# Kernel tuning notes

Measured on AMD Instinct MI355X. Metric: run time of the kernel, lower is better.

The kernel has to match this reference:

```python
import jax, jax.numpy as jnp
import numpy as np

NATTRS, NOBJS = 250, 400
N = NATTRS + NOBJS           # 650 graph nodes
E = 100000                   # edges
D_IN, D_HID, D_NODE = 512, 4096, 512
FEAT, EMB, B = 2048, 800, 256
LN_EPS = 1e-5


def setup_inputs() -> dict:
    key = jax.random.key(0)
    ks = jax.random.split(key, 32)
    w = lambda k, shape: (jax.random.normal(k, shape, jnp.float32) / np.sqrt(shape[-1])).astype(jnp.float32)
    return {
        'img': jax.random.normal(ks[0], (B, FEAT), jnp.float32),
        'nodes': jax.random.normal(ks[1], (N, D_IN), jnp.float32),
        'edge_src': jax.random.randint(ks[2], (E,), 0, N),
        'edge_dst': jax.random.randint(ks[3], (E,), 0, N),
        'W1l': w(ks[4], (D_HID, D_IN)), 'b1': jnp.zeros((D_HID,), jnp.float32), 'W1r': w(ks[5], (D_HID, D_IN)),
        'W2l': w(ks[6], (D_NODE, D_HID)), 'b2': jnp.zeros((D_NODE,), jnp.float32), 'W2r': w(ks[7], (D_NODE, D_HID)),
        'Wp1': w(ks[8], (1200, 2 * D_NODE)), 'bp1': jnp.zeros((1200,), jnp.float32),
        'Wp2': w(ks[9], (EMB, 1200)), 'bp2': jnp.zeros((EMB,), jnp.float32),
        'gp': jnp.ones((EMB,), jnp.float32), 'bpn': jnp.zeros((EMB,), jnp.float32),
        'Wi1': w(ks[10], (768, FEAT)), 'bi1': jnp.zeros((768,), jnp.float32),
        'Wi2': w(ks[11], (1000, 768)), 'bi2': jnp.zeros((1000,), jnp.float32),
        'Wi3': w(ks[12], (EMB, 1000)), 'bi3': jnp.zeros((EMB,), jnp.float32),
        'gi': jnp.ones((EMB,), jnp.float32), 'bin_': jnp.zeros((EMB,), jnp.float32),
    }


def _segment_mean(x, src, dst, n):
    # gather source features, mean-aggregate at destinations (PyG SAGEConv 'mean')
    agg = jax.ops.segment_sum(x[src], dst, num_segments=n)
    deg = jax.ops.segment_sum(jnp.ones_like(dst, dtype=x.dtype), dst, num_segments=n)
    return agg / jnp.clip(deg, 1.0)[:, None]


def _sage(x, src, dst, Wl, bl, Wr):
    # out_i = lin_l(mean_{j in N(i)} x_j) + lin_r(x_i); lin_r has no bias in PyG
    return _segment_mean(x, src, dst, x.shape[0]) @ Wl.T + bl + x @ Wr.T


def _ln(x, g, b):
    m = x.mean(-1, keepdims=True)
    v = ((x - m) ** 2).mean(-1, keepdims=True)
    return (x - m) / jnp.sqrt(v + LN_EPS) * g + b


def reference(img, nodes, edge_src, edge_dst, W1l, b1, W1r, W2l, b2, W2r,
              Wp1, bp1, Wp2, bp2, gp, bpn, Wi1, bi1, Wi2, bi2, Wi3, bi3, gi, bin_):
    # GCN backbone (dropout is identity in eval)
    h = jax.nn.relu(_sage(nodes, edge_src, edge_dst, W1l, b1, W1r))
    out_nodes = _sage(h, edge_src, edge_dst, W2l, b2, W2r)          # [N, 512]
    # all attr-obj pairs: attr repeated per obj, objs tiled per attr
    attr = out_nodes[:NATTRS]
    obj = out_nodes[NATTRS:]
    pa = jnp.repeat(attr, NOBJS, axis=0)                            # [P, 512]
    po = jnp.tile(obj, (NATTRS, 1))                                 # [P, 512]
    pairs = jnp.concatenate([pa, po], axis=1)                       # [P, 1024]
    # pair_fc: Linear-ReLU -> Linear -> LayerNorm
    p = jax.nn.relu(pairs @ Wp1.T + bp1)
    p = _ln(p @ Wp2.T + bp2, gp, bpn)                               # [P, 800]
    # img_fc: two hidden Linear-ReLU -> Linear -> LayerNorm
    i = jax.nn.relu(img @ Wi1.T + bi1)
    i = jax.nn.relu(i @ Wi2.T + bi2)
    i = _ln(i @ Wi3.T + bi3, gi, bin_)                              # [B, 800]
    return i @ p.T                                                  # [B, P]
```

## Files before the change

### kernel.cpp

```cpp
#include <hip/hip_runtime.h>

#define NN 650
#define NE 100000

typedef short bf16x8_t __attribute__((ext_vector_type(8)));
typedef short s16x4_t __attribute__((ext_vector_type(4)));
typedef float f32x4_t __attribute__((ext_vector_type(4)));

__device__ __forceinline__ unsigned short f2bf(float f) {
  union { float f; unsigned u; } x; x.f = f;
  unsigned r = x.u + 0x7fffu + ((x.u >> 16) & 1u);
  return (unsigned short)(r >> 16);
}
__device__ __forceinline__ float bf2f(unsigned short u) {
  union { unsigned u; float f; } x; x.u = ((unsigned)u) << 16; return x.f;
}

typedef const __attribute__((address_space(1))) unsigned int* gptr_t;
typedef __attribute__((address_space(3))) unsigned int* lptr_t;
__device__ __forceinline__ void gl_lds16(const unsigned short* g, unsigned short* l) {
  __builtin_amdgcn_global_load_lds((gptr_t)g, (lptr_t)l, 16, 0, 0);
}

__global__ void k_scatter(const int* __restrict__ src, const int* __restrict__ dst,
                          float* __restrict__ C, float* __restrict__ deg) {
  int e = blockIdx.x * 256 + threadIdx.x;
  if (e < NE) {
    int s = src[e], d = dst[e];
    atomicAdd(&C[d * NN + s], 1.0f);
    atomicAdd(&deg[d], 1.0f);
  }
}

__global__ void k_adj_norm(const float* __restrict__ C, const float* __restrict__ deg,
                           unsigned short* __restrict__ Cn) {
  int idx = blockIdx.x * 256 + threadIdx.x;
  if (idx >= 768 * 672) return;
  int i = idx / 672, j = idx - i * 672;
  float v = (i < NN && j < NN) ? C[i * NN + j] / fmaxf(deg[i], 1.0f) : 0.0f;
  Cn[idx] = f2bf(v);
}

#define MAXJ 12
struct CvtDesc { const float* src; unsigned short* dst; int Mvalid, Kin, ldi, off, ldo, nElem, nblk; };
struct CvtPack { CvtDesc d[MAXJ]; };
__global__ void k_cvt_all(CvtPack P) {
  int b = blockIdx.x;
  int j = 0;
  while (b >= P.d[j].nblk) { b -= P.d[j].nblk; ++j; }
  const CvtDesc D = P.d[j];
  int idx = b * 256 + threadIdx.x;
  if (idx >= D.nElem) return;
  int r = idx / D.ldo, c = idx - r * D.ldo;
  D.dst[idx] = (r < D.Mvalid && c < D.Kin) ? f2bf(D.src[(size_t)r * D.ldi + D.off + c]) : (unsigned short)0;
}

__global__ void k_ttr(const unsigned short* __restrict__ in, unsigned short* __restrict__ out,
                      int ldi, int ldo) {
  __shared__ unsigned short tile[64][65];
  const int c0 = blockIdx.x * 64, r0 = blockIdx.y * 64;
  const int t = threadIdx.x;
  const int rl = t >> 4, cl = (t & 15) * 4;
#pragma unroll
  for (int rr = 0; rr < 4; ++rr) {
    s16x4_t v = *(const s16x4_t*)(in + (size_t)(r0 + rl + rr * 16) * ldi + c0 + cl);
#pragma unroll
    for (int j = 0; j < 4; ++j) tile[rl + rr * 16][cl + j] = (unsigned short)v[j];
  }
  __syncthreads();
  if (r0 + cl < ldo) {
#pragma unroll
    for (int cc = 0; cc < 4; ++cc) {
      int crow = rl + cc * 16;
      unsigned short o[4] = { tile[cl + 0][crow], tile[cl + 1][crow],
                              tile[cl + 2][crow], tile[cl + 3][crow] };
      *(s16x4_t*)(out + (size_t)(c0 + crow) * ldo + r0 + cl) = *(s16x4_t*)o;
    }
  }
}

__global__ void k_pgen(const float* __restrict__ Pa, const float* __restrict__ Po,
                       unsigned short* __restrict__ P, int r0, int rows) {
  int g = blockIdx.x * 256 + threadIdx.x;
  if (g >= rows * 152) return;
  int lp = g / 152, k = (g - lp * 152) * 8;
  int p = r0 + lp;
  unsigned short t8[8];
  if (p < 100000) {
    int a = p / 400, o = p - a * 400;
    const float* pa = Pa + (size_t)a * 1216 + k;
    const float* po = Po + (size_t)o * 1216 + k;
    float4 x1 = *(const float4*)(pa);
    float4 x2 = *(const float4*)(pa + 4);
    float4 y1 = *(const float4*)(po);
    float4 y2 = *(const float4*)(po + 4);
    t8[0] = f2bf(fmaxf(x1.x + y1.x, 0.f)); t8[1] = f2bf(fmaxf(x1.y + y1.y, 0.f));
    t8[2] = f2bf(fmaxf(x1.z + y1.z, 0.f)); t8[3] = f2bf(fmaxf(x1.w + y1.w, 0.f));
    t8[4] = f2bf(fmaxf(x2.x + y2.x, 0.f)); t8[5] = f2bf(fmaxf(x2.y + y2.y, 0.f));
    t8[6] = f2bf(fmaxf(x2.z + y2.z, 0.f)); t8[7] = f2bf(fmaxf(x2.w + y2.w, 0.f));
  } else {
#pragma unroll
    for (int j = 0; j < 8; ++j) t8[j] = 0;
  }
  *(bf16x8_t*)(P + (size_t)lp * 1216 + k) = *(bf16x8_t*)t8;
}

__global__ void k_stats_fin(float* __restrict__ S, float* __restrict__ SS) {
  int i = blockIdx.x * 256 + threadIdx.x;
  if (i >= 100096) return;
  float s = S[i], ss = SS[i];
  float m = s * (1.0f / 800.0f);
  float var = ss * (1.0f / 800.0f) - m * m;
  S[i] = m;
  SS[i] = rsqrtf(fmaxf(var, 0.f) + 1e-5f);
}

__global__ void k_prep_i(const unsigned short* __restrict__ iB,
                         const float* __restrict__ gp, const float* __restrict__ bpn,
                         unsigned short* __restrict__ iG,
                         float* __restrict__ c1, float* __restrict__ c2) {
  const int row = blockIdx.x, t = threadIdx.x;
  float s1 = 0.f, s2 = 0.f;
  if (t < 100) {
    bf16x8_t v = *(const bf16x8_t*)(iB + (size_t)row * 800 + t * 8);
    unsigned short o[8];
#pragma unroll
    for (int j = 0; j < 8; ++j) {
      float f = bf2f((unsigned short)v[j]);
      float g = gp[t * 8 + j];
      s1 += f * g; s2 += f * bpn[t * 8 + j];
      o[j] = f2bf(f * g);
    }
    *(bf16x8_t*)(iG + (size_t)row * 800 + t * 8) = *(bf16x8_t*)o;
  }
#pragma unroll
  for (int off = 32; off > 0; off >>= 1) { s1 += __shfl_down(s1, off); s2 += __shfl_down(s2, off); }
  __shared__ float sh[4];
  int w = t >> 6, lane = t & 63;
  if (lane == 0) { sh[w] = s1; sh[2 + w] = s2; }
  __syncthreads();
  if (t == 0) { c1[row] = sh[0] + sh[1]; c2[row] = sh[2] + sh[3]; }
}

#define BK 32
template<int OUT_BF, int RELU, int LNF, int QST>
__launch_bounds__(256)
__global__ void k_gemm128(const unsigned short* __restrict__ A,
                          const unsigned short* __restrict__ B,
                          const float* __restrict__ bias,
                          const float* __restrict__ addb,
                          void* __restrict__ Cout,
                          int K, int ldc,
                          int Mvalid, int Nvalid, int Nstore, int swap, int swz,
                          const float* __restrict__ lnm, const float* __restrict__ lninv,
                          const float* __restrict__ lnc1, const float* __restrict__ lnc2,
                          float* __restrict__ sumP, float* __restrict__ ssP) {
  __shared__ unsigned short As[2][128 * BK];
  __shared__ unsigned short Bs[2][128 * BK];
  const int tid = threadIdx.x;
  const int w = tid >> 6, lane = tid & 63;
  int bx = blockIdx.x, by = blockIdx.y;
  if (swz) {
    int T = gridDim.x * gridDim.y;
    int flat = blockIdx.x + gridDim.x * blockIdx.y;
    int xcd = flat & 7, s = flat >> 3;
    int qq = T >> 3, rr = T & 7;
    int slot = (xcd < rr ? xcd * (qq + 1) : rr * (qq + 1) + (xcd - rr) * qq) + s;
    bx = slot % gridDim.x; by = slot / gridDim.x;
  }
  const int bm = swap ? by : bx;
  const int bn = swap ? bx : by;
  const int m0 = bm * 128, n0 = bn * 128;
  const int wm = w & 1, wn = w >> 1;
  const int lr = lane & 15, q = lane >> 4;

  const int srow = w * 32 + (lane >> 2);
  const int scol = (lane & 3) * 8;
  const unsigned short* Ag = A + (size_t)(m0 + srow) * K + scol;
  const unsigned short* Bg = B + (size_t)(n0 + srow) * K + scol;
  const int so0 = (w * 32) * BK;
  const int so1 = (w * 32 + 16) * BK;

  f32x4_t acc[4][4];
#pragma unroll
  for (int r = 0; r < 4; ++r)
#pragma unroll
    for (int t = 0; t < 4; ++t) { f32x4_t z = {0.f, 0.f, 0.f, 0.f}; acc[r][t] = z; }

  const int nt = K / BK;
  gl_lds16(Ag, &As[0][so0]); gl_lds16(Ag + 16 * (size_t)K, &As[0][so1]);
  gl_lds16(Bg, &Bs[0][so0]); gl_lds16(Bg + 16 * (size_t)K, &Bs[0][so1]);
  Ag += BK; Bg += BK;

  for (int t = 0; t < nt; ++t) {
    const int cur = t & 1;
    __syncthreads();
    if (t + 1 < nt) {
      const int nxt = cur ^ 1;
      gl_lds16(Ag, &As[nxt][so0]); gl_lds16(Ag + 16 * (size_t)K, &As[nxt][so1]);
      gl_lds16(Bg, &Bs[nxt][so0]); gl_lds16(Bg + 16 * (size_t)K, &Bs[nxt][so1]);
      Ag += BK; Bg += BK;
    }
    bf16x8_t af[4], bfv[4];
#pragma unroll
    for (int r = 0; r < 4; ++r)
      af[r] = *(const bf16x8_t*)(&As[cur][(wm * 64 + r * 16 + lr) * BK + q * 8]);
#pragma unroll
    for (int tt = 0; tt < 4; ++tt)
      bfv[tt] = *(const bf16x8_t*)(&Bs[cur][(wn * 64 + tt * 16 + lr) * BK + q * 8]);
#pragma unroll
    for (int r = 0; r < 4; ++r)
#pragma unroll
      for (int tt = 0; tt < 4; ++tt)
        acc[r][tt] = __builtin_amdgcn_mfma_f32_16x16x32_bf16(af[r], bfv[tt], acc[r][tt], 0, 0, 0);
  }

  if (QST) {
#pragma unroll
    for (int r = 0; r < 4; ++r) {
#pragma unroll
      for (int e = 0; e < 4; ++e) {
        const int gm = m0 + wm * 64 + r * 16 + q * 4 + e;
        float s = 0.f, ss = 0.f;
#pragma unroll
        for (int t = 0; t < 4; ++t) {
          const int gn = n0 + wn * 64 + t * 16 + lr;
          float v = 0.f;
          if (gm < Mvalid && gn < Nvalid) v = acc[r][t][e] + bias[gn];
          if (gn < Nstore)
            ((unsigned short*)Cout)[(size_t)gm * ldc + gn] = f2bf(v);
          s += v; ss += v * v;
        }
#pragma unroll
        for (int m = 1; m < 16; m <<= 1) {
          s += __shfl_xor(s, m);
          ss += __shfl_xor(ss, m);
        }
        if (lr == 0 && gm < Mvalid) {
          atomicAdd(&sumP[gm], s);
          atomicAdd(&ssP[gm], ss);
        }
      }
    }
  } else {
#pragma unroll
    for (int r = 0; r < 4; ++r) {
#pragma unroll
      for (int t = 0; t < 4; ++t) {
#pragma unroll
        for (int e = 0; e < 4; ++e) {
          int gm = m0 + wm * 64 + r * 16 + q * 4 + e;
          int gn = n0 + wn * 64 + t * 16 + lr;
          if (gn < Nstore) {
            float v = 0.f;
            if (gm < Mvalid && gn < Nvalid) {
              v = acc[r][t][e];
              if (LNF) {
                v = lninv[gn] * (v - lnm[gn] * lnc1[gm]) + lnc2[gm];
              } else {
                if (bias) v += bias[gn];
                if (addb) v += addb[(size_t)gm * ldc + gn];
                if (RELU) v = fmaxf(v, 0.f);
              }
            }
            if (OUT_BF) ((unsigned short*)Cout)[(size_t)gm * ldc + gn] = f2bf(v);
            else        ((float*)Cout)[(size_t)gm * ldc + gn] = v;
          }
        }
      }
    }
  }
}

__global__ void k_ln_img(const float* __restrict__ in, unsigned short* __restrict__ out,
                         const float* __restrict__ g, const float* __restrict__ b) {
  const int row = blockIdx.x, t = threadIdx.x;
  float v[4]; float s = 0.f, ss = 0.f; int j = 0;
  for (int idx = t; idx < 800; idx += 256, ++j) {
    float x = in[(size_t)row * 800 + idx];
    v[j] = x; s += x; ss += x * x;
  }
#pragma unroll
  for (int off = 32; off > 0; off >>= 1) {
    s += __shfl_down(s, off);
    ss += __shfl_down(ss, off);
  }
  __shared__ float sh[8];
  int wave = t >> 6, lane = t & 63;
  if (lane == 0) { sh[wave] = s; sh[4 + wave] = ss; }
  __syncthreads();
  if (t == 0) {
    float S = sh[0] + sh[1] + sh[2] + sh[3];
    float SS = sh[4] + sh[5] + sh[6] + sh[7];
    float m = S * (1.0f / 800.0f);
    float var = SS * (1.0f / 800.0f) - m * m;
    sh[0] = m; sh[1] = rsqrtf(fmaxf(var, 0.f) + 1e-5f);
  }
  __syncthreads();
  float m = sh[0], inv = sh[1];
  j = 0;
  for (int idx = t; idx < 800; idx += 256, ++j) {
    float y = (v[j] - m) * inv * g[idx] + b[idx];
    out[(size_t)row * 800 + idx] = f2bf(y);
  }
}

extern "C" void kernel_launch(void* const* d_in, const int* in_sizes, int n_in,
                              void* d_out, int out_size, void* d_ws, size_t ws_size,
                              hipStream_t stream) {
  (void)in_sizes; (void)n_in; (void)out_size; (void)ws_size;
  const float* img  = (const float*)d_in[0];
  const float* nodes= (const float*)d_in[1];
  const int* esrc   = (const int*)d_in[2];
  const int* edst   = (const int*)d_in[3];
  const float* W1l  = (const float*)d_in[4];
  const float* b1   = (const float*)d_in[5];
  const float* W1r  = (const float*)d_in[6];
  const float* W2l  = (const float*)d_in[7];
  const float* b2   = (const float*)d_in[8];
  const float* W2r  = (const float*)d_in[9];
  const float* Wp1  = (const float*)d_in[10];
  const float* bp1  = (const float*)d_in[11];
  const float* Wp2  = (const float*)d_in[12];
  const float* bp2  = (const float*)d_in[13];
  const float* gp   = (const float*)d_in[14];
  const float* bpn  = (const float*)d_in[15];
  const float* Wi1  = (const float*)d_in[16];
  const float* bi1  = (const float*)d_in[17];
  const float* Wi2  = (const float*)d_in[18];
  const float* bi2  = (const float*)d_in[19];
  const float* Wi3  = (const float*)d_in[20];
  const float* bi3  = (const float*)d_in[21];
  const float* gi   = (const float*)d_in[22];
  const float* binp = (const float*)d_in[23];

  char* wsp = (char*)d_ws;
  auto alloc = [&](size_t bytes) -> void* {
    void* p = (void*)wsp; wsp += (bytes + 255) & ~(size_t)255; return p;
  };
  unsigned short* onB    = (unsigned short*)alloc((size_t)768 * 512 * 2);
  unsigned short* Wp1LB  = (unsigned short*)alloc((size_t)1280 * 512 * 2);
  unsigned short* Wp1RB  = (unsigned short*)alloc((size_t)1280 * 512 * 2);
  unsigned short* Wp2B   = (unsigned short*)alloc((size_t)896 * 1216 * 2);
  float* PaB             = (float*)alloc((size_t)256 * 1216 * 4);
  float* PoB             = (float*)alloc((size_t)512 * 1216 * 4);
  unsigned short* imgB   = (unsigned short*)alloc((size_t)256 * 2048 * 2);
  unsigned short* Wi1B   = (unsigned short*)alloc((size_t)768 * 2048 * 2);
  unsigned short* Wi2B   = (unsigned short*)alloc((size_t)1024 * 768 * 2);
  unsigned short* Wi3B   = (unsigned short*)alloc((size_t)896 * 1024 * 2);
  unsigned short* i1B    = (unsigned short*)alloc((size_t)256 * 768 * 2);
  unsigned short* i2B    = (unsigned short*)alloc((size_t)256 * 1024 * 2);
  float* i3F             = (float*)alloc((size_t)256 * 800 * 4);
  unsigned short* iB     = (unsigned short*)alloc((size_t)256 * 800 * 2);
  unsigned short* iG     = (unsigned short*)alloc((size_t)256 * 800 * 2);
  float* c1B             = (float*)alloc(256 * 4);
  float* c2B             = (float*)alloc(256 * 4);
  float* mArr            = (float*)alloc((size_t)100096 * 4);
  float* ivArr           = (float*)alloc((size_t)100096 * 4);
  unsigned short* qB     = (unsigned short*)alloc((size_t)100096 * 800 * 2);

  char* swp = (char*)qB;
  auto salloc = [&](size_t bytes) -> void* {
    void* p = (void*)swp; swp += (bytes + 255) & ~(size_t)255; return p;
  };
  float* adjC            = (float*)salloc((size_t)NN * NN * 4);
  float* deg             = (float*)salloc(NN * 4);
  unsigned short* Cn     = (unsigned short*)salloc((size_t)768 * 672 * 2);
  unsigned short* nodesB = (unsigned short*)salloc((size_t)768 * 512 * 2);
  unsigned short* nodesT = (unsigned short*)salloc((size_t)512 * 672 * 2);
  unsigned short* agg1   = (unsigned short*)salloc((size_t)768 * 512 * 2);
  float* tmp1            = (float*)salloc((size_t)768 * 4096 * 4);
  unsigned short* hB     = (unsigned short*)salloc((size_t)768 * 4096 * 2);
  unsigned short* hT     = (unsigned short*)salloc((size_t)4096 * 672 * 2);
  unsigned short* agg2   = (unsigned short*)salloc((size_t)768 * 4096 * 2);
  float* tmp2            = (float*)salloc((size_t)768 * 512 * 4);
  unsigned short* W1lB   = (unsigned short*)salloc((size_t)4096 * 512 * 2);
  unsigned short* W1rB   = (unsigned short*)salloc((size_t)4096 * 512 * 2);
  unsigned short* W2lB   = (unsigned short*)salloc((size_t)512 * 4096 * 2);
  unsigned short* W2rB   = (unsigned short*)salloc((size_t)512 * 4096 * 2);

  unsigned short* Pch = (unsigned short*)d_out;

  hipMemsetAsync(adjC, 0, (size_t)NN * NN * 4, stream);
  hipMemsetAsync(deg, 0, NN * 4, stream);
  hipMemsetAsync(mArr, 0, (size_t)100096 * 4, stream);
  hipMemsetAsync(ivArr, 0, (size_t)100096 * 4, stream);

  k_scatter<<<dim3((NE + 255) / 256), 256, 0, stream>>>(esrc, edst, adjC, deg);
  k_adj_norm<<<dim3((768 * 672 + 255) / 256), 256, 0, stream>>>(adjC, deg, Cn);

  {
    CvtPack pk; int nj = 0, tot = 0;
    auto addj = [&](const float* s, unsigned short* d, int Mv, int Mp, int Kin, int ldi, int off, int ldo) {
      int ne = Mp * ldo, nb = (ne + 255) / 256;
      pk.d[nj++] = { s, d, Mv, Kin, ldi, off, ldo, ne, nb };
      tot += nb;
    };
    addj(nodes, nodesB, 650, 768, 512, 512, 0, 512);
    addj(W1l, W1lB, 4096, 4096, 512, 512, 0, 512);
    addj(W1r, W1rB, 4096, 4096, 512, 512, 0, 512);
    addj(W2l, W2lB, 512, 512, 4096, 4096, 0, 4096);
    addj(W2r, W2rB, 512, 512, 4096, 4096, 0, 4096);
    addj(Wp1, Wp1LB, 1200, 1280, 512, 1024, 0, 512);
    addj(Wp1, Wp1RB, 1200, 1280, 512, 1024, 512, 512);
    addj(Wp2, Wp2B, 800, 896, 1200, 1200, 0, 1216);
    addj(Wi1, Wi1B, 768, 768, 2048, 2048, 0, 2048);
    addj(Wi2, Wi2B, 1000, 1024, 768, 768, 0, 768);
    addj(Wi3, Wi3B, 800, 896, 1000, 1000, 0, 1024);
    addj(img, imgB, 256, 256, 2048, 2048, 0, 2048);
    k_cvt_all<<<dim3(tot), 256, 0, stream>>>(pk);
  }

  k_ttr<<<dim3(512 / 64, (672 + 63) / 64), 256, 0, stream>>>(nodesB, nodesT, 512, 672);

#define NUL nullptr, nullptr, nullptr, nullptr, nullptr, nullptr
  k_gemm128<1, 0, 0, 0><<<dim3(6, 4), 256, 0, stream>>>(Cn, nodesT, nullptr, nullptr, agg1, 672, 512, 650, 512, 512, 0, 0, NUL);
  k_gemm128<0, 0, 0, 0><<<dim3(6, 32), 256, 0, stream>>>(agg1, W1lB, b1, nullptr, tmp1, 512, 4096, 650, 4096, 4096, 0, 0, NUL);
  k_gemm128<1, 1, 0, 0><<<dim3(6, 32), 256, 0, stream>>>(nodesB, W1rB, nullptr, tmp1, hB, 512, 4096, 650, 4096, 4096, 0, 0, NUL);
  k_ttr<<<dim3(4096 / 64, (672 + 63) / 64), 256, 0, stream>>>(hB, hT, 4096, 672);
  k_gemm128<1, 0, 0, 0><<<dim3(6, 32), 256, 0, stream>>>(Cn, hT, nullptr, nullptr, agg2, 672, 4096, 650, 4096, 4096, 0, 0, NUL);
  k_gemm128<0, 0, 0, 0><<<dim3(6, 4), 256, 0, stream>>>(agg2, W2lB, b2, nullptr, tmp2, 4096, 512, 650, 512, 512, 0, 0, NUL);
  k_gemm128<1, 0, 0, 0><<<dim3(6, 4), 256, 0, stream>>>(hB, W2rB, nullptr, tmp2, onB, 4096, 512, 650, 512, 512, 0, 0, NUL);
  k_gemm128<0, 0, 0, 0><<<dim3(2, 10), 256, 0, stream>>>(onB, Wp1LB, bp1, nullptr, PaB, 512, 1216, 250, 1200, 1216, 0, 0, NUL);
  k_gemm128<0, 0, 0, 0><<<dim3(4, 10), 256, 0, stream>>>(onB + 250 * 512, Wp1RB, nullptr, nullptr, PoB, 512, 1216, 400, 1200, 1216, 0, 0, NUL);

  k_gemm128<1, 1, 0, 0><<<dim3(2, 6), 256, 0, stream>>>(imgB, Wi1B, bi1, nullptr, i1B, 2048, 768, 256, 768, 768, 0, 0, NUL);
  k_gemm128<1, 1, 0, 0><<<dim3(2, 8), 256, 0, stream>>>(i1B, Wi2B, bi2, nullptr, i2B, 768, 1024, 256, 1000, 1024, 0, 0, NUL);
  k_gemm128<0, 0, 0, 0><<<dim3(2, 7), 256, 0, stream>>>(i2B, Wi3B, bi3, nullptr, i3F, 1024, 800, 256, 800, 800, 0, 0, NUL);
  k_ln_img<<<dim3(256), 256, 0, stream>>>(i3F, iB, gi, binp);
  k_prep_i<<<dim3(256), 128, 0, stream>>>(iB, gp, bpn, iG, c1B, c2B);

  const int CB = 262;
  for (int c = 0; c < 3; ++c) {
    int b0 = c * CB;
    int nb = (782 - b0) < CB ? (782 - b0) : CB;
    int r0 = b0 * 128;
    int rows = nb * 128;
    k_pgen<<<dim3((rows * 152 + 255) / 256), 256, 0, stream>>>(PaB, PoB, Pch, r0, rows);
    int mv = (100000 - r0) < rows ? (100000 - r0) : rows;
    k_gemm128<1, 0, 0, 1><<<dim3(7, nb), 256, 0, stream>>>(Pch, Wp2B, bp2, nullptr,
        qB + (size_t)r0 * 800, 1216, 800, mv, 800, 800, 1, 1,
        nullptr, nullptr, nullptr, nullptr, mArr + r0, ivArr + r0);
  }
  k_stats_fin<<<dim3((100096 + 255) / 256), 256, 0, stream>>>(mArr, ivArr);

  k_gemm128<0, 0, 1, 0><<<dim3(2, 782), 256, 0, stream>>>(iG, qB, nullptr, nullptr, (float*)d_out,
      800, 100000, 256, 100000, 100000, 0, 1, mArr, ivArr, c1B, c2B, nullptr, nullptr);
#undef NUL
}
```

Baseline: 1.301 ms.

## Add split-K atomics for small-grid GEMMs and XOR-swizzle LDS tiles

Adds a split-K template path that divides the K dimension across gridDim.z and accumulates partial results into zeroed fp32 buffers with atomicAdd. Separate finalize kernels then apply bias, ReLU and the bf16 conversion. This is used for the deep-K, few-tile GEMMs (W2 layers and the image MLP), which previously launched only 14 to 24 blocks. It also XOR-swizzles the LDS tile column offsets on both the store and the fragment read, to reduce bank conflicts in every GEMM. The cost is extra memsets, atomics traffic, finalize launches and non-deterministic summation order.

```diff
diff --git a/kernel.cpp b/kernel.cpp
--- a/kernel.cpp
+++ b/kernel.cpp
@@ -115,6 +115,23 @@
   SS[i] = rsqrtf(fmaxf(var, 0.f) + 1e-5f);
 }
 
+__global__ void k_fin_on(const float* __restrict__ acc, const float* __restrict__ bias,
+                         unsigned short* __restrict__ out) {
+  int i = blockIdx.x * 256 + threadIdx.x;
+  if (i >= 768 * 512) return;
+  int r = i >> 9, c = i & 511;
+  out[i] = f2bf(r < 650 ? acc[i] + bias[c] : 0.f);
+}
+__global__ void k_fin_rb(const float* __restrict__ acc, const float* __restrict__ bias,
+                         unsigned short* __restrict__ out, int nElem, int cols, int Nv) {
+  int i = blockIdx.x * 256 + threadIdx.x;
+  if (i >= nElem) return;
+  int c = i % cols;
+  float v = 0.f;
+  if (c < Nv) v = fmaxf(acc[i] + bias[c], 0.f);
+  out[i] = f2bf(v);
+}
+
 __global__ void k_prep_i(const unsigned short* __restrict__ iB,
                          const float* __restrict__ gp, const float* __restrict__ bpn,
                          unsigned short* __restrict__ iG,
@@ -143,7 +160,7 @@
 }
 
 #define BK 32
-template<int OUT_BF, int RELU, int LNF, int QST>
+template<int OUT_BF, int RELU, int LNF, int QST, int SK>
 __launch_bounds__(256)
 __global__ void k_gemm128(const unsigned short* __restrict__ A,
                           const unsigned short* __restrict__ B,
@@ -175,9 +192,16 @@
   const int lr = lane & 15, q = lane >> 4;
 
   const int srow = w * 32 + (lane >> 2);
-  const int scol = (lane & 3) * 8;
-  const unsigned short* Ag = A + (size_t)(m0 + srow) * K + scol;
-  const unsigned short* Bg = B + (size_t)(n0 + srow) * K + scol;
+  const int mw_ = ((lane >> 2) & 3) ^ ((lane >> 4) & 3);
+  const int scol = (((lane & 3) ^ mw_) * 8);
+  const int mr_ = (lane & 3) ^ ((lane >> 2) & 3);
+  const int qe = ((q ^ mr_) * 8);
+
+  int nt = K / BK, kt0 = 0;
+  if (SK) { int Ksl = K / (int)gridDim.z; nt = Ksl / BK; kt0 = blockIdx.z * (Ksl / BK); }
+
+  const unsigned short* Ag = A + (size_t)(m0 + srow) * K + (size_t)kt0 * BK + scol;
+  const unsigned short* Bg = B + (size_t)(n0 + srow) * K + (size_t)kt0 * BK + scol;
   const int so0 = (w * 32) * BK;
   const int so1 = (w * 32 + 16) * BK;
 
@@ -187,7 +211,6 @@
 #pragma unroll
     for (int t = 0; t < 4; ++t) { f32x4_t z = {0.f, 0.f, 0.f, 0.f}; acc[r][t] = z; }
 
-  const int nt = K / BK;
   gl_lds16(Ag, &As[0][so0]); gl_lds16(Ag + 16 * (size_t)K, &As[0][so1]);
   gl_lds16(Bg, &Bs[0][so0]); gl_lds16(Bg + 16 * (size_t)K, &Bs[0][so1]);
   Ag += BK; Bg += BK;
@@ -204,10 +227,10 @@
     bf16x8_t af[4], bfv[4];
 #pragma unroll
     for (int r = 0; r < 4; ++r)
-      af[r] = *(const bf16x8_t*)(&As[cur][(wm * 64 + r * 16 + lr) * BK + q * 8]);
+      af[r] = *(const bf16x8_t*)(&As[cur][(wm * 64 + r * 16 + lr) * BK + qe]);
 #pragma unroll
     for (int tt = 0; tt < 4; ++tt)
-      bfv[tt] = *(const bf16x8_t*)(&Bs[cur][(wn * 64 + tt * 16 + lr) * BK + q * 8]);
+      bfv[tt] = *(const bf16x8_t*)(&Bs[cur][(wn * 64 + tt * 16 + lr) * BK + qe]);
 #pragma unroll
     for (int r = 0; r < 4; ++r)
 #pragma unroll
@@ -215,7 +238,19 @@
         acc[r][tt] = __builtin_amdgcn_mfma_f32_16x16x32_bf16(af[r], bfv[tt], acc[r][tt], 0, 0, 0);
   }
 
-  if (QST) {
+  if (SK) {
+#pragma unroll
+    for (int r = 0; r < 4; ++r)
+#pragma unroll
+      for (int t = 0; t < 4; ++t)
+#pragma unroll
+        for (int e = 0; e < 4; ++e) {
+          int gm = m0 + wm * 64 + r * 16 + q * 4 + e;
+          int gn = n0 + wn * 64 + t * 16 + lr;
+          if (gm < Mvalid && gn < Nvalid)
+            atomicAdd((float*)Cout + (size_t)gm * ldc + gn, acc[r][t][e]);
+        }
+  } else if (QST) {
 #pragma unroll
     for (int r = 0; r < 4; ++r) {
 #pragma unroll
@@ -272,12 +307,13 @@
   }
 }
 
-__global__ void k_ln_img(const float* __restrict__ in, unsigned short* __restrict__ out,
+__global__ void k_ln_img(const float* __restrict__ in, const float* __restrict__ bb,
+                         unsigned short* __restrict__ out,
                          const float* __restrict__ g, const float* __restrict__ b) {
   const int row = blockIdx.x, t = threadIdx.x;
   float v[4]; float s = 0.f, ss = 0.f; int j = 0;
   for (int idx = t; idx < 800; idx += 256, ++j) {
-    float x = in[(size_t)row * 800 + idx];
+    float x = in[(size_t)row * 800 + idx] + bb[idx];
     v[j] = x; s += x; ss += x * x;
   }
 #pragma unroll
@@ -378,6 +414,8 @@
   unsigned short* W1rB   = (unsigned short*)salloc((size_t)4096 * 512 * 2);
   unsigned short* W2lB   = (unsigned short*)salloc((size_t)512 * 4096 * 2);
   unsigned short* W2rB   = (unsigned short*)salloc((size_t)512 * 4096 * 2);
+  float* F1              = (float*)salloc((size_t)256 * 768 * 4);
+  float* F2              = (float*)salloc((size_t)256 * 1024 * 4);
 
   unsigned short* Pch = (unsigned short*)d_out;
 
@@ -385,6 +423,10 @@
   hipMemsetAsync(deg, 0, NN * 4, stream);
   hipMemsetAsync(mArr, 0, (size_t)100096 * 4, stream);
   hipMemsetAsync(ivArr, 0, (size_t)100096 * 4, stream);
+  hipMemsetAsync(tmp2, 0, (size_t)768 * 512 * 4, stream);
+  hipMemsetAsync(F1, 0, (size_t)256 * 768 * 4, stream);
+  hipMemsetAsync(F2, 0, (size_t)256 * 1024 * 4, stream);
+  hipMemsetAsync(i3F, 0, (size_t)256 * 800 * 4, stream);
 
   k_scatter<<<dim3((NE + 255) / 256), 256, 0, stream>>>(esrc, edst, adjC, deg);
   k_adj_norm<<<dim3((768 * 672 + 255) / 256), 256, 0, stream>>>(adjC, deg, Cn);
@@ -414,20 +456,23 @@
   k_ttr<<<dim3(512 / 64, (672 + 63) / 64), 256, 0, stream>>>(nodesB, nodesT, 512, 672);
 
 #define NUL nullptr, nullptr, nullptr, nullptr, nullptr, nullptr
-  k_gemm128<1, 0, 0, 0><<<dim3(6, 4), 256, 0, stream>>>(Cn, nodesT, nullptr, nullptr, agg1, 672, 512, 650, 512, 512, 0, 0, NUL);
-  k_gemm128<0, 0, 0, 0><<<dim3(6, 32), 256, 0, stream>>>(agg1, W1lB, b1, nullptr, tmp1, 512, 4096, 650, 4096, 4096, 0, 0, NUL);
-  k_gemm128<1, 1, 0, 0><<<dim3(6, 32), 256, 0, stream>>>(nodesB, W1rB, nullptr, tmp1, hB, 512, 4096, 650, 4096, 4096, 0, 0, NUL);
+  k_gemm128<1, 0, 0, 0, 0><<<dim3(6, 4), 256, 0, stream>>>(Cn, nodesT, nullptr, nullptr, agg1, 672, 512, 650, 512, 512, 0, 0, NUL);
+  k_gemm128<0, 0, 0, 0, 0><<<dim3(6, 32), 256, 0, stream>>>(agg1, W1lB, b1, nullptr, tmp1, 512, 4096, 650, 4096, 4096, 0, 0, NUL);
+  k_gemm128<1, 1, 0, 0, 0><<<dim3(6, 32), 256, 0, stream>>>(nodesB, W1rB, nullptr, tmp1, hB, 512, 4096, 650, 4096, 4096, 0, 0, NUL);
   k_ttr<<<dim3(4096 / 64, (672 + 63) / 64), 256, 0, stream>>>(hB, hT, 4096, 672);
-  k_gemm128<1, 0, 0, 0><<<dim3(6, 32), 256, 0, stream>>>(Cn, hT, nullptr, nullptr, agg2, 672, 4096, 650, 4096, 4096, 0, 0, NUL);
-  k_gemm128<0, 0, 0, 0><<<dim3(6, 4), 256, 0, stream>>>(agg2, W2lB, b2, nullptr, tmp2, 4096, 512, 650, 512, 512, 0, 0, NUL);
-  k_gemm128<1, 0, 0, 0><<<dim3(6, 4), 256, 0, stream>>>(hB, W2rB, nullptr, tmp2, onB, 4096, 512, 650, 512, 512, 0, 0, NUL);
-  k_gemm128<0, 0, 0, 0><<<dim3(2, 10), 256, 0, stream>>>(onB, Wp1LB, bp1, nullptr, PaB, 512, 1216, 250, 1200, 1216, 0, 0, NUL);
-  k_gemm128<0, 0, 0, 0><<<dim3(4, 10), 256, 0, stream>>>(onB + 250 * 512, Wp1RB, nullptr, nullptr, PoB, 512, 1216, 400, 1200, 1216, 0, 0, NUL);
-
-  k_gemm128<1, 1, 0, 0><<<dim3(2, 6), 256, 0, stream>>>(imgB, Wi1B, bi1, nullptr, i1B, 2048, 768, 256, 768, 768, 0, 0, NUL);
-  k_gemm128<1, 1, 0, 0><<<dim3(2, 8), 256, 0, stream>>>(i1B, Wi2B, bi2, nullptr, i2B, 768, 1024, 256, 1000, 1024, 0, 0, NUL);
-  k_gemm128<0, 0, 0, 0><<<dim3(2, 7), 256, 0, stream>>>(i2B, Wi3B, bi3, nullptr, i3F, 1024, 800, 256, 800, 800, 0, 0, NUL);
-  k_ln_img<<<dim3(256), 256, 0, stream>>>(i3F, iB, gi, binp);
+  k_gemm128<1, 0, 0, 0, 0><<<dim3(6, 32), 256, 0, stream>>>(Cn, hT, nullptr, nullptr, agg2, 672, 4096, 650, 4096, 4096, 0, 0, NUL);
+  k_gemm128<0, 0, 0, 0, 1><<<dim3(6, 4, 8), 256, 0, stream>>>(agg2, W2lB, nullptr, nullptr, tmp2, 4096, 512, 650, 512, 512, 0, 0, NUL);
+  k_gemm128<0, 0, 0, 0, 1><<<dim3(6, 4, 8), 256, 0, stream>>>(hB, W2rB, nullptr, nullptr, tmp2, 4096, 512, 650, 512, 512, 0, 0, NUL);
+  k_fin_on<<<dim3((768 * 512 + 255) / 256), 256, 0, stream>>>(tmp2, b2, onB);
+  k_gemm128<0, 0, 0, 0, 0><<<dim3(2, 10), 256, 0, stream>>>(onB, Wp1LB, bp1, nullptr, PaB, 512, 1216, 250, 1200, 1216, 0, 0, NUL);
+  k_gemm128<0, 0, 0, 0, 0><<<dim3(4, 10), 256, 0, stream>>>(onB + 250 * 512, Wp1RB, nullptr, nullptr, PoB, 512, 1216, 400, 1200, 1216, 0, 0, NUL);
+
+  k_gemm128<0, 0, 0, 0, 1><<<dim3(2, 6, 8), 256, 0, stream>>>(imgB, Wi1B, nullptr, nullptr, F1, 2048, 768, 256, 768, 768, 0, 0, NUL);
+  k_fin_rb<<<dim3((256 * 768 + 255) / 256), 256, 0, stream>>>(F1, bi1, i1B, 256 * 768, 768, 768);
+  k_gemm128<0, 0, 0, 0, 1><<<dim3(2, 8, 8), 256, 0, stream>>>(i1B, Wi2B, nullptr, nullptr, F2, 768, 1024, 256, 1000, 1024, 0, 0, NUL);
+  k_fin_rb<<<dim3((256 * 1024 + 255) / 256), 256, 0, stream>>>(F2, bi2, i2B, 256 * 1024, 1024, 1000);
+  k_gemm128<0, 0, 0, 0, 1><<<dim3(2, 7, 8), 256, 0, stream>>>(i2B, Wi3B, nullptr, nullptr, i3F, 1024, 800, 256, 800, 800, 0, 0, NUL);
+  k_ln_img<<<dim3(256), 256, 0, stream>>>(i3F, bi3, iB, gi, binp);
   k_prep_i<<<dim3(256), 128, 0, stream>>>(iB, gp, bpn, iG, c1B, c2B);
 
   const int CB = 262;
@@ -438,13 +483,13 @@
     int rows = nb * 128;
     k_pgen<<<dim3((rows * 152 + 255) / 256), 256, 0, stream>>>(PaB, PoB, Pch, r0, rows);
     int mv = (100000 - r0) < rows ? (100000 - r0) : rows;
-    k_gemm128<1, 0, 0, 1><<<dim3(7, nb), 256, 0, stream>>>(Pch, Wp2B, bp2, nullptr,
+    k_gemm128<1, 0, 0, 1, 0><<<dim3(7, nb), 256, 0, stream>>>(Pch, Wp2B, bp2, nullptr,
         qB + (size_t)r0 * 800, 1216, 800, mv, 800, 800, 1, 1,
         nullptr, nullptr, nullptr, nullptr, mArr + r0, ivArr + r0);
   }
   k_stats_fin<<<dim3((100096 + 255) / 256), 256, 0, stream>>>(mArr, ivArr);
 
-  k_gemm128<0, 0, 1, 0><<<dim3(2, 782), 256, 0, stream>>>(iG, qB, nullptr, nullptr, (float*)d_out,
+  k_gemm128<0, 0, 1, 0, 0><<<dim3(2, 782), 256, 0, stream>>>(iG, qB, nullptr, nullptr, (float*)d_out,
       800, 100000, 256, 100000, 100000, 0, 1, mArr, ivArr, c1B, c2B, nullptr, nullptr);
 #undef NUL
 }
```

New measurement: 1.094 ms. 1.19x faster.
